# Kernel tuning notes

Hardware: AMD Instinct MI355X
Metric: run time of the kernel (lower is better)

Reference implementation:

```python
import jax, jax.numpy as jnp
import numpy as np
import math

B, T = 16, 60
N_CLASSES = 80
N_ANCHORS = 3
N_CH = 5 + N_CLASSES
STRIDES = (8, 16, 32)
IMG = 608
ANCHORS = np.array([[12,16],[19,36],[40,28],[36,75],[76,55],[72,146],[142,110],[192,243],[459,401]], dtype=np.float32)
IGNORE_THRE = 0.5


def _clip_log(x):
    # torch F.binary_cross_entropy clamps log at -100
    return jnp.maximum(jnp.log(x), -100.0)


def _bce_sum(p, t, w=None):
    l = -(t * _clip_log(p) + (1.0 - t) * _clip_log(1.0 - p))
    if w is not None:
        l = l * w
    return jnp.sum(l)


def _ciou_wh(wh_a, wh_b):
    # truth boxes are xyxy [0,0,w,h]; wh_a [B,T,2], wh_b [9,2] -> CIoU [B,T,9]
    wa = wh_a[..., 0:1]; ha = wh_a[..., 1:2]
    wb = wh_b[:, 0];     hb = wh_b[:, 1]
    iw = jnp.minimum(wa, wb); ih = jnp.minimum(ha, hb)
    en = ((iw > 0) & (ih > 0)).astype(wh_a.dtype)
    area_i = iw * ih * en
    area_u = wa * ha + wb * hb - area_i
    iou = area_i / area_u
    c2 = jnp.maximum(wa, wb) ** 2 + jnp.maximum(ha, hb) ** 2 + 1e-16
    rho2 = ((wa - wb) ** 2 + (ha - hb) ** 2) / 4.0
    v = (4.0 / math.pi ** 2) * (jnp.arctan(wa / ha) - jnp.arctan(wb / hb)) ** 2
    alpha = v / (1.0 - iou + v)
    return iou - (rho2 / c2 + v * alpha)


def _iou_xywh(pred, truth):
    # pred [B,N,4] (cx,cy,w,h), truth [B,T,4] -> IoU [B,N,T]
    p_xy = pred[:, :, None, :2]; p_wh = pred[:, :, None, 2:]
    t_xy = truth[:, None, :, :2]; t_wh = truth[:, None, :, 2:]
    tl = jnp.maximum(p_xy - p_wh * 0.5, t_xy - t_wh * 0.5)
    br = jnp.minimum(p_xy + p_wh * 0.5, t_xy + t_wh * 0.5)
    en = jnp.all(tl < br, axis=-1).astype(pred.dtype)
    area_i = jnp.prod(br - tl, axis=-1) * en
    area_p = pred[..., 2] * pred[..., 3]
    area_t = truth[..., 2] * truth[..., 3]
    return area_i / (area_p[:, :, None] + area_t[:, None, :] - area_i)


def _level_losses(x, labels, oid):
    dt = x.dtype
    stride = STRIDES[oid]
    fsize = IMG // stride
    Bsz = x.shape[0]
    out = x.reshape(Bsz, N_ANCHORS, N_CH, fsize, fsize).transpose(0, 1, 3, 4, 2)  # [B,A,F,F,C]
    sig = jax.nn.sigmoid(out)
    sxy, raw_wh, sobj, scls = sig[..., :2], out[..., 2:4], sig[..., 4], sig[..., 5:]

    all_anch = jnp.asarray(ANCHORS / stride, dt)           # [9,2] grid units
    masked_anch = all_anch[3 * oid: 3 * oid + 3]           # [3,2]
    g = jnp.arange(fsize, dtype=dt)
    px = sxy[..., 0] + g[None, None, None, :]
    py = sxy[..., 1] + g[None, None, :, None]
    pw = jnp.exp(raw_wh[..., 0]) * masked_anch[:, 0][None, :, None, None]
    ph = jnp.exp(raw_wh[..., 1]) * masked_anch[:, 1][None, :, None, None]
    pred = jnp.stack([px, py, pw, ph], axis=-1)            # [B,A,F,F,4]

    lab = jax.lax.stop_gradient(labels.astype(dt))         # targets carry no grad (as in torch)
    valid = jnp.sum(lab, axis=-1) > 0                      # [B,T]
    tx = (lab[..., 2] + lab[..., 0]) / (stride * 2.0)
    ty = (lab[..., 3] + lab[..., 1]) / (stride * 2.0)
    tw = (lab[..., 2] - lab[..., 0]) / stride
    th = (lab[..., 3] - lab[..., 1]) / stride
    ii = jnp.clip(tx.astype(jnp.int32), 0, fsize - 1)      # int16 trunc in torch, coords >= 0
    jj = jnp.clip(ty.astype(jnp.int32), 0, fsize - 1)

    ciou = _ciou_wh(jnp.stack([tw, th], -1), all_anch)     # [B,T,9]
    ciou = jnp.where(valid[..., None], ciou, -1e9)
    best_all = jnp.argmax(ciou, axis=-1)                   # [B,T]
    best_n = best_all % 3
    best_mask = (best_all // 3 == oid) & valid             # anchor owned by this level
    has_match = jnp.any(best_mask, axis=1)                 # [B]; torch `continue` if none

    truth_box = jnp.stack([tx, ty, tw, th], -1) * valid[..., None].astype(dt)
    ious = _iou_xywh(jax.lax.stop_gradient(pred).reshape(Bsz, -1, 4), truth_box)
    ious = jnp.where(valid[:, None, :], ious, 0.0)
    ignore = (jnp.max(ious, axis=-1) > IGNORE_THRE).reshape(Bsz, N_ANCHORS, fsize, fsize)
    obj_mask = jnp.where(has_match[:, None, None, None], 1.0 - ignore.astype(dt), jnp.asarray(1.0, dt))

    # scatter positive assignments; dummy batch row Bsz absorbs masked-out writes
    bidx = jnp.where(best_mask, jnp.arange(Bsz, dtype=jnp.int32)[:, None], Bsz)
    pad1 = lambda a: jnp.concatenate([a, jnp.zeros((1,) + a.shape[1:], a.dtype)], 0)
    obj_mask = pad1(obj_mask).at[bidx, best_n, jj, ii].set(1.0)[:Bsz]
    tgt_mask = jnp.zeros((Bsz + 1, N_ANCHORS, fsize, fsize, 4 + N_CLASSES), dt).at[bidx, best_n, jj, ii].set(1.0)[:Bsz]
    scale = jnp.sqrt(2.0 - tw * th / float(fsize * fsize))  # [B,T]
    tgt_scale = jnp.zeros((Bsz + 1, N_ANCHORS, fsize, fsize, 2), dt).at[bidx, best_n, jj, ii].set(
        jnp.broadcast_to(scale[..., None], scale.shape + (2,)))[:Bsz]
    aw = masked_anch[best_n, 0]; ah = masked_anch[best_n, 1]
    vec = jnp.concatenate([
        (tx - jnp.trunc(tx))[..., None],
        (ty - jnp.trunc(ty))[..., None],
        jnp.log(tw / aw + 1e-16)[..., None],
        jnp.log(th / ah + 1e-16)[..., None],
        jnp.ones_like(tx)[..., None],
        jax.nn.one_hot(lab[..., 4].astype(jnp.int32), N_CLASSES, dtype=dt),
    ], axis=-1)                                            # [B,T,N_CH]
    target = jnp.zeros((Bsz + 1, N_ANCHORS, fsize, fsize, N_CH), dt).at[bidx, best_n, jj, ii].set(vec)[:Bsz]

    o_xy = sxy * tgt_mask[..., :2]
    o_wh = raw_wh * tgt_mask[..., 2:4] * tgt_scale
    o_obj = sobj * obj_mask
    o_cls = scls * tgt_mask[..., 4:]
    t_xy = target[..., :2] * tgt_mask[..., :2]
    t_wh = target[..., 2:4] * tgt_mask[..., 2:4] * tgt_scale
    t_obj = target[..., 4] * obj_mask
    t_cls = target[..., 5:] * tgt_mask[..., 4:]

    l_xy = _bce_sum(o_xy, t_xy, tgt_scale * tgt_scale)
    l_wh = 0.5 * jnp.sum((o_wh - t_wh) ** 2)
    l_obj = _bce_sum(o_obj, t_obj)
    l_cls = _bce_sum(o_cls, t_cls)
    l_l2 = (jnp.sum((o_xy - t_xy) ** 2) + jnp.sum((o_wh - t_wh) ** 2)
            + jnp.sum((o_obj - t_obj) ** 2) + jnp.sum((o_cls - t_cls) ** 2))
    return l_xy, l_wh, l_obj, l_cls, l_l2


def setup_inputs() -> dict:
    key = jax.random.key(0)
    ks = jax.random.split(key, 8)
    x0 = jax.random.normal(ks[0], (B, N_ANCHORS * N_CH, 76, 76), jnp.float32)
    x1 = jax.random.normal(ks[1], (B, N_ANCHORS * N_CH, 38, 38), jnp.float32)
    x2 = jax.random.normal(ks[2], (B, N_ANCHORS * N_CH, 19, 19), jnp.float32)
    cx = jax.random.uniform(ks[3], (B, T), minval=70.0, maxval=538.0)
    cy = jax.random.uniform(ks[4], (B, T), minval=70.0, maxval=538.0)
    bw = jax.random.uniform(ks[5], (B, T), minval=8.0, maxval=128.0)
    bh = jax.random.uniform(ks[6], (B, T), minval=8.0, maxval=128.0)
    cls = jax.random.randint(ks[7], (B, T), 0, N_CLASSES).astype(jnp.float32)
    labels = jnp.stack([cx - bw / 2, cy - bh / 2, cx + bw / 2, cy + bh / 2, cls], axis=-1)
    nvalid = jax.random.randint(jax.random.fold_in(key, 99), (B,), 5, T + 1)
    mask = (jnp.arange(T)[None, :] < nvalid[:, None]).astype(jnp.float32)
    labels = labels * mask[..., None]  # zero padding rows (nlabel = rows with sum>0)
    return {"x0": x0, "x1": x1, "x2": x2, "labels": labels}


def reference(x0, x1, x2, labels):
    totals = [jnp.asarray(0.0, x0.dtype)] * 5
    for oid, x in enumerate((x0, x1, x2)):
        parts = _level_losses(x, labels, oid)
        totals = [a + b for a, b in zip(totals, parts)]
    l_xy, l_wh, l_obj, l_cls, l_l2 = totals
    loss = l_xy + l_wh + l_obj + l_cls
    return loss, l_xy, l_wh, l_obj, l_cls, l_l2
```

## Files before the change

kernel.cpp:

```cpp
#include <hip/hip_runtime.h>

#define BATCH 16
#define TT 60
#define NCLS 80
#define NB0 68
#define NB1 17
#define NB2 5
#define NBX (NB0 + NB1 + NB2)
#define NBLK (NBX * BATCH)

__constant__ float c_aw[9] = {12.f,19.f,40.f,36.f,76.f,72.f,142.f,192.f,459.f};
__constant__ float c_ah[9] = {16.f,36.f,28.f,75.f,55.f,146.f,110.f,243.f,401.f};

__device__ __forceinline__ float sigf(float x){ return 1.0f/(1.0f+expf(-x)); }
__device__ __forceinline__ float clogf_(float x){ return fmaxf(logf(x), -100.0f); }
__device__ __forceinline__ float bcef(float p, float t){
    return -(t*clogf_(p) + (1.0f-t)*clogf_(1.0f-p));
}

__global__ __launch_bounds__(256) void main_kernel(
    const float* __restrict__ x0, const float* __restrict__ x1,
    const float* __restrict__ x2, const float* __restrict__ labels,
    float* __restrict__ ws)
{
    const int bx = blockIdx.x, b = blockIdx.y, tid = threadIdx.x;
    int lvl, lb, fs;
    const float* x;
    if (bx < NB0)            { lvl = 0; lb = bx;             x = x0; fs = 76; }
    else if (bx < NB0 + NB1) { lvl = 1; lb = bx - NB0;       x = x1; fs = 38; }
    else                     { lvl = 2; lb = bx - NB0 - NB1; x = x2; fs = 19; }
    const float stride = (float)(8 << lvl);
    const float invs = 1.0f/stride;
    const int fs2 = fs*fs;
    const int ncell = 3*fs2;
    const int lin = lb*256 + tid;

    __shared__ float  s_atan[9];
    __shared__ float4 s_box[TT];
    __shared__ int    s_mcell[TT], s_mcls[TT];
    __shared__ float  s_vx[TT], s_vy[TT], s_vw[TT], s_vh[TT], s_sc[TT];
    __shared__ int    s_nv, s_nm, s_qn;
    __shared__ int    s_qoff[TT], s_qcls[TT];

    float v0=0,v1=0,v2=0,v3=0,v4=0;
    int a=0, rem=0, ci=0, cj=0;
    if (lin < ncell) {
        a = lin/fs2; rem = lin - a*fs2; cj = rem/fs; ci = rem - cj*fs;
        const float* xb = x + ((size_t)b*255 + a*85)*(size_t)fs2 + rem;
        v0 = xb[0];
        v1 = xb[(size_t)fs2];
        v2 = xb[(size_t)2*fs2];
        v3 = xb[(size_t)3*fs2];
        v4 = xb[(size_t)4*fs2];
    }
    float l0=0,l1=0,l2=0,l3=0,l4=0;
    if (tid < TT) {
        const float* lab = labels + ((size_t)b*TT + tid)*5;
        l0=lab[0]; l1=lab[1]; l2=lab[2]; l3=lab[3]; l4=lab[4];
    }
    if (tid < 9) s_atan[tid] = atanf(c_aw[tid]/c_ah[tid]);
    if (tid == 0) s_qn = 0;
    __syncthreads();

    if (tid < 64) {
        bool valid=false, best=false;
        float tx=0,ty=0,tw=0,th=0;
        int best_all=0;
        if (tid < TT) {
            valid = ((((l0+l1)+l2)+l3)+l4) > 0.0f;
            tx = (l2+l0)*(0.5f*invs);
            ty = (l3+l1)*(0.5f*invs);
            tw = (l2-l0)*invs;
            th = (l3-l1)*invs;
            if (valid) {
                float ta = atanf(tw/th);
                float twth = tw*th;
                float bestv = 0.0f;
                for (int k=0;k<9;k++){
                    float wb=c_aw[k]*invs, hb=c_ah[k]*invs;
                    float iw=fminf(tw,wb), ih=fminf(th,hb);
                    float en=(iw>0.f && ih>0.f)?1.f:0.f;
                    float ai=iw*ih*en;
                    float au=twth+wb*hb-ai;
                    float iou=ai/au;
                    float mw=fmaxf(tw,wb), mh=fmaxf(th,hb);
                    float c2=mw*mw+mh*mh+1e-16f;
                    float rho2=((tw-wb)*(tw-wb)+(th-hb)*(th-hb))*0.25f;
                    float da=ta-s_atan[k];
                    float v=0.40528473456935109f*da*da;
                    float alpha=v/((1.f-iou)+v);
                    float cv=iou-(rho2/c2+v*alpha);
                    if (k==0 || cv>bestv){ bestv=cv; best_all=k; }
                }
            }
        }
        int bn = best_all % 3;
        best = valid && ((best_all/3) == lvl);
        unsigned long long vm = __ballot(valid);
        unsigned long long bm = __ballot(best);
        unsigned long long below = (tid==0) ? 0ULL : ((1ULL<<tid)-1ULL);
        if (valid){
            int r = __popcll(vm & below);
            s_box[r] = make_float4(tx-0.5f*tw, ty-0.5f*th, tx+0.5f*tw, ty+0.5f*th);
        }
        if (best){
            int r = __popcll(bm & below);
            int ti=(int)tx, tj=(int)ty;
            int ii = ti<0?0:(ti>fs-1?fs-1:ti);
            int jj = tj<0?0:(tj>fs-1?fs-1:tj);
            s_mcell[r] = (bn*fs+jj)*fs+ii;
            s_mcls[r]  = (int)l4;
            s_sc[r]    = sqrtf(2.f - tw*th/(float)(fs*fs));
            s_vx[r]    = tx - truncf(tx);
            s_vy[r]    = ty - truncf(ty);
            float aw = c_aw[3*lvl+bn]*invs, ah = c_ah[3*lvl+bn]*invs;
            s_vw[r]    = logf(tw/aw + 1e-16f);
            s_vh[r]    = logf(th/ah + 1e-16f);
        }
        if (tid==0){ s_nv = __popcll(vm); s_nm = __popcll(bm); }
    }
    __syncthreads();

    const int nv = s_nv, nm = s_nm;
    float lxy=0.f, lwh=0.f, lobj=0.f, lcls=0.f, ll2=0.f;
    if (lin < ncell) {
        const float sx = sigf(v0), sy = sigf(v1), sobj = sigf(v4);
        const float aw = c_aw[3*lvl+a]*invs, ah = c_ah[3*lvl+a]*invs;
        const float px = sx + (float)ci;
        const float py = sy + (float)cj;
        const float pw = expf(v2)*aw;
        const float ph = expf(v3)*ah;
        const float area_p = pw*ph;

        int mt = -1;
        for (int k=0;k<nm;k++) if (s_mcell[k] == lin) mt = k;

        bool ign = false;
        if (nm > 0 && mt < 0) {
            const float pxl = px-0.5f*pw, pxr = px+0.5f*pw;
            const float pyl = py-0.5f*ph, pyr = py+0.5f*ph;
            #pragma unroll 4
            for (int t=0;t<nv;t++){
                float4 tb = s_box[t];
                float w = fminf(pxr,tb.z) - fmaxf(pxl,tb.x);
                float h = fminf(pyr,tb.w) - fmaxf(pyl,tb.y);
                float at2 = (tb.z-tb.x)*(tb.w-tb.y);
                ign = ign || ((w>0.f)&&(h>0.f)&&(3.f*(w*h) > area_p+at2));
            }
        }
        float om = (nm>0) ? (ign ? 0.f : 1.f) : 1.f;
        float t4 = 0.f;
        if (mt >= 0){ om = 1.f; t4 = 1.f; }
        const float oo = sobj*om, to = t4*om;
        lobj = bcef(oo, to);
        const float d = oo - to;
        ll2 = d*d;
        if (mt >= 0) {
            const float sc = s_sc[mt], w2 = sc*sc;
            const float mvx = s_vx[mt], mvy = s_vy[mt];
            lxy = w2*(bcef(sx,mvx) + bcef(sy,mvy));
            const float dx = sx-mvx, dy = sy-mvy;
            const float dw = sc*(v2 - s_vw[mt]);
            const float dh = sc*(v3 - s_vh[mt]);
            lwh = 0.5f*(dw*dw + dh*dh);
            ll2 += dx*dx + dy*dy + dw*dw + dh*dh;
            int qi = atomicAdd(&s_qn, 1);
            s_qoff[qi] = (a*85+5)*fs2 + rem;
            s_qcls[qi] = s_mcls[mt];
        }
    }
    __syncthreads();

    const int wid = tid>>6, ln = tid&63;
    const int qn = s_qn;
    for (int it = wid; it < qn; it += 4){
        const size_t base = (size_t)b*255*(size_t)fs2 + (size_t)s_qoff[it];
        const int cc = s_qcls[it];
        float p = sigf(x[base + (size_t)ln*fs2]);
        float tt = (ln==cc) ? 1.f : 0.f;
        lcls += bcef(p, tt);
        float dd = p - tt; ll2 += dd*dd;
        if (ln < NCLS-64) {
            int c = 64+ln;
            p = sigf(x[base + (size_t)c*fs2]);
            tt = (c==cc) ? 1.f : 0.f;
            lcls += bcef(p, tt);
            dd = p - tt; ll2 += dd*dd;
        }
    }

    for (int off=32; off>0; off>>=1){
        lxy  += __shfl_down(lxy,  off);
        lwh  += __shfl_down(lwh,  off);
        lobj += __shfl_down(lobj, off);
        lcls += __shfl_down(lcls, off);
        ll2  += __shfl_down(ll2,  off);
    }
    __shared__ float red[4][5];
    if (ln == 0){ red[wid][0]=lxy; red[wid][1]=lwh; red[wid][2]=lobj; red[wid][3]=lcls; red[wid][4]=ll2; }
    __syncthreads();
    if (tid == 0){
        const int blk = b*NBX + bx;
        ws[0*NBLK + blk] = red[0][0]+red[1][0]+red[2][0]+red[3][0];
        ws[1*NBLK + blk] = red[0][1]+red[1][1]+red[2][1]+red[3][1];
        ws[2*NBLK + blk] = red[0][2]+red[1][2]+red[2][2]+red[3][2];
        ws[3*NBLK + blk] = red[0][3]+red[1][3]+red[2][3]+red[3][3];
        ws[4*NBLK + blk] = red[0][4]+red[1][4]+red[2][4]+red[3][4];
    }
}

__global__ __launch_bounds__(256) void fin_kernel(const float* __restrict__ ws, float* __restrict__ out){
    const int tid = threadIdx.x;
    float s[5] = {0.f,0.f,0.f,0.f,0.f};
    for (int i = tid; i < NBLK; i += 256){
        #pragma unroll
        for (int c=0;c<5;c++) s[c] += ws[c*NBLK + i];
    }
    for (int off=32; off>0; off>>=1){
        #pragma unroll
        for (int c=0;c<5;c++) s[c] += __shfl_down(s[c], off);
    }
    __shared__ float red[4][5];
    const int wid = tid >> 6, ln = tid & 63;
    if (ln == 0){ for (int c=0;c<5;c++) red[wid][c] = s[c]; }
    __syncthreads();
    if (tid == 0){
        float t_xy  = red[0][0]+red[1][0]+red[2][0]+red[3][0];
        float t_wh  = red[0][1]+red[1][1]+red[2][1]+red[3][1];
        float t_obj = red[0][2]+red[1][2]+red[2][2]+red[3][2];
        float t_cls = red[0][3]+red[1][3]+red[2][3]+red[3][3];
        float t_l2  = red[0][4]+red[1][4]+red[2][4]+red[3][4];
        out[0] = t_xy + t_wh + t_obj + t_cls;
        out[1] = t_xy; out[2] = t_wh; out[3] = t_obj; out[4] = t_cls; out[5] = t_l2;
    }
}

extern "C" void kernel_launch(void* const* d_in, const int* in_sizes, int n_in,
                              void* d_out, int out_size, void* d_ws, size_t ws_size,
                              hipStream_t stream) {
    const float* x0 = (const float*)d_in[0];
    const float* x1 = (const float*)d_in[1];
    const float* x2 = (const float*)d_in[2];
    const float* labels = (const float*)d_in[3];
    float* out = (float*)d_out;
    float* ws = (float*)d_ws;

    main_kernel<<<dim3(NBX, BATCH), 256, 0, stream>>>(x0, x1, x2, labels, ws);
    fin_kernel<<<1, 256, 0, stream>>>(ws, out);
}
```

Before: 28.57 us.

## Process two cells per thread and fuse final reduction via last-block atomics

Each thread now handles two grid cells, which halves the block count and amortises the per-block label matching and shared-memory setup over twice as many cells. The separate finalize kernel is replaced by float atomics into the workspace plus a last-block counter that writes the outputs, with a memset to zero the accumulators. This trades a kernel launch for a memset and float atomic ordering. Float atomics make the summation order nondeterministic, and the ignore loop now also runs for matched cells.

Result: slower. 72.53 us (+153.9%).

```diff
diff --git a/kernel.cpp b/kernel.cpp
--- a/kernel.cpp
+++ b/kernel.cpp
@@ -3,11 +3,11 @@
 #define BATCH 16
 #define TT 60
 #define NCLS 80
-#define NB0 68
-#define NB1 17
-#define NB2 5
+#define NB0 34
+#define NB1 9
+#define NB2 3
 #define NBX (NB0 + NB1 + NB2)
-#define NBLK (NBX * BATCH)
+#define NBLK_TOT (NBX * BATCH)
 
 __constant__ float c_aw[9] = {12.f,19.f,40.f,36.f,76.f,72.f,142.f,192.f,459.f};
 __constant__ float c_ah[9] = {16.f,36.f,28.f,75.f,55.f,146.f,110.f,243.f,401.f};
@@ -21,7 +21,7 @@
 __global__ __launch_bounds__(256) void main_kernel(
     const float* __restrict__ x0, const float* __restrict__ x1,
     const float* __restrict__ x2, const float* __restrict__ labels,
-    float* __restrict__ ws)
+    float* __restrict__ ws, float* __restrict__ out)
 {
     const int bx = blockIdx.x, b = blockIdx.y, tid = threadIdx.x;
     int lvl, lb, fs;
@@ -29,29 +29,32 @@
     if (bx < NB0)            { lvl = 0; lb = bx;             x = x0; fs = 76; }
     else if (bx < NB0 + NB1) { lvl = 1; lb = bx - NB0;       x = x1; fs = 38; }
     else                     { lvl = 2; lb = bx - NB0 - NB1; x = x2; fs = 19; }
-    const float stride = (float)(8 << lvl);
-    const float invs = 1.0f/stride;
+    const float invs = 1.0f/(float)(8 << lvl);
     const int fs2 = fs*fs;
     const int ncell = 3*fs2;
-    const int lin = lb*256 + tid;
+    const int lin0 = lb*512 + tid;
+    const int lin1 = lin0 + 256;
 
     __shared__ float  s_atan[9];
     __shared__ float4 s_box[TT];
     __shared__ int    s_mcell[TT], s_mcls[TT];
     __shared__ float  s_vx[TT], s_vy[TT], s_vw[TT], s_vh[TT], s_sc[TT];
-    __shared__ int    s_nv, s_nm, s_qn;
+    __shared__ int    s_nv, s_nm, s_qn, s_last;
     __shared__ int    s_qoff[TT], s_qcls[TT];
 
-    float v0=0,v1=0,v2=0,v3=0,v4=0;
-    int a=0, rem=0, ci=0, cj=0;
-    if (lin < ncell) {
-        a = lin/fs2; rem = lin - a*fs2; cj = rem/fs; ci = rem - cj*fs;
-        const float* xb = x + ((size_t)b*255 + a*85)*(size_t)fs2 + rem;
-        v0 = xb[0];
-        v1 = xb[(size_t)fs2];
-        v2 = xb[(size_t)2*fs2];
-        v3 = xb[(size_t)3*fs2];
-        v4 = xb[(size_t)4*fs2];
+    float v0a=0,v1a=0,v2a=0,v3a=0,v4a=0, v0b=0,v1b=0,v2b=0,v3b=0,v4b=0;
+    int a0=0,rem0=0,ci0=0,cj0=0, a1=0,rem1=0,ci1=0,cj1=0;
+    if (lin0 < ncell) {
+        a0 = lin0/fs2; rem0 = lin0 - a0*fs2; cj0 = rem0/fs; ci0 = rem0 - cj0*fs;
+        const float* xb = x + ((size_t)b*255 + a0*85)*(size_t)fs2 + rem0;
+        v0a = xb[0]; v1a = xb[(size_t)fs2]; v2a = xb[(size_t)2*fs2];
+        v3a = xb[(size_t)3*fs2]; v4a = xb[(size_t)4*fs2];
+    }
+    if (lin1 < ncell) {
+        a1 = lin1/fs2; rem1 = lin1 - a1*fs2; cj1 = rem1/fs; ci1 = rem1 - cj1*fs;
+        const float* xb = x + ((size_t)b*255 + a1*85)*(size_t)fs2 + rem1;
+        v0b = xb[0]; v1b = xb[(size_t)fs2]; v2b = xb[(size_t)2*fs2];
+        v3b = xb[(size_t)3*fs2]; v4b = xb[(size_t)4*fs2];
     }
     float l0=0,l1=0,l2=0,l3=0,l4=0;
     if (tid < TT) {
@@ -123,50 +126,84 @@
 
     const int nv = s_nv, nm = s_nm;
     float lxy=0.f, lwh=0.f, lobj=0.f, lcls=0.f, ll2=0.f;
-    if (lin < ncell) {
-        const float sx = sigf(v0), sy = sigf(v1), sobj = sigf(v4);
-        const float aw = c_aw[3*lvl+a]*invs, ah = c_ah[3*lvl+a]*invs;
-        const float px = sx + (float)ci;
-        const float py = sy + (float)cj;
-        const float pw = expf(v2)*aw;
-        const float ph = expf(v3)*ah;
-        const float area_p = pw*ph;
-
-        int mt = -1;
-        for (int k=0;k<nm;k++) if (s_mcell[k] == lin) mt = k;
-
-        bool ign = false;
-        if (nm > 0 && mt < 0) {
-            const float pxl = px-0.5f*pw, pxr = px+0.5f*pw;
-            const float pyl = py-0.5f*ph, pyr = py+0.5f*ph;
+    const bool c0 = (lin0 < ncell), c1 = (lin1 < ncell);
+    if (c0 | c1) {
+        const float sxa = sigf(v0a), sya = sigf(v1a), soa = sigf(v4a);
+        const float sxb = sigf(v0b), syb = sigf(v1b), sob = sigf(v4b);
+        const float awa = c_aw[3*lvl+a0]*invs, aha = c_ah[3*lvl+a0]*invs;
+        const float awb = c_aw[3*lvl+a1]*invs, ahb = c_ah[3*lvl+a1]*invs;
+        const float pxa = sxa + (float)ci0, pya = sya + (float)cj0;
+        const float pxb = sxb + (float)ci1, pyb = syb + (float)cj1;
+        const float pwa = expf(v2a)*awa, pha = expf(v3a)*aha;
+        const float pwb = expf(v2b)*awb, phb = expf(v3b)*ahb;
+        const float apa = pwa*pha, apb = pwb*phb;
+
+        int mt0 = -1, mt1 = -1;
+        for (int k=0;k<nm;k++){
+            int mc = s_mcell[k];
+            if (mc == lin0) mt0 = k;
+            if (mc == lin1) mt1 = k;
+        }
+
+        bool iga = false, igb = false;
+        if (nm > 0) {
+            const float xla = pxa-0.5f*pwa, xra = pxa+0.5f*pwa;
+            const float yla = pya-0.5f*pha, yra = pya+0.5f*pha;
+            const float xlb = pxb-0.5f*pwb, xrb = pxb+0.5f*pwb;
+            const float ylb = pyb-0.5f*phb, yrb = pyb+0.5f*phb;
             #pragma unroll 4
             for (int t=0;t<nv;t++){
                 float4 tb = s_box[t];
-                float w = fminf(pxr,tb.z) - fmaxf(pxl,tb.x);
-                float h = fminf(pyr,tb.w) - fmaxf(pyl,tb.y);
                 float at2 = (tb.z-tb.x)*(tb.w-tb.y);
-                ign = ign || ((w>0.f)&&(h>0.f)&&(3.f*(w*h) > area_p+at2));
-            }
-        }
-        float om = (nm>0) ? (ign ? 0.f : 1.f) : 1.f;
-        float t4 = 0.f;
-        if (mt >= 0){ om = 1.f; t4 = 1.f; }
-        const float oo = sobj*om, to = t4*om;
-        lobj = bcef(oo, to);
-        const float d = oo - to;
-        ll2 = d*d;
-        if (mt >= 0) {
-            const float sc = s_sc[mt], w2 = sc*sc;
-            const float mvx = s_vx[mt], mvy = s_vy[mt];
-            lxy = w2*(bcef(sx,mvx) + bcef(sy,mvy));
-            const float dx = sx-mvx, dy = sy-mvy;
-            const float dw = sc*(v2 - s_vw[mt]);
-            const float dh = sc*(v3 - s_vh[mt]);
-            lwh = 0.5f*(dw*dw + dh*dh);
-            ll2 += dx*dx + dy*dy + dw*dw + dh*dh;
-            int qi = atomicAdd(&s_qn, 1);
-            s_qoff[qi] = (a*85+5)*fs2 + rem;
-            s_qcls[qi] = s_mcls[mt];
+                float wa = fminf(xra,tb.z) - fmaxf(xla,tb.x);
+                float ha = fminf(yra,tb.w) - fmaxf(yla,tb.y);
+                float wb = fminf(xrb,tb.z) - fmaxf(xlb,tb.x);
+                float hb = fminf(yrb,tb.w) - fmaxf(ylb,tb.y);
+                iga = iga || ((wa>0.f)&&(ha>0.f)&&(3.f*(wa*ha) > apa+at2));
+                igb = igb || ((wb>0.f)&&(hb>0.f)&&(3.f*(wb*hb) > apb+at2));
+            }
+        }
+        if (c0) {
+            float om = (nm>0) ? (iga ? 0.f : 1.f) : 1.f;
+            float t4 = 0.f;
+            if (mt0 >= 0){ om = 1.f; t4 = 1.f; }
+            float oo = soa*om, to = t4*om;
+            lobj += bcef(oo, to);
+            float d = oo - to; ll2 += d*d;
+            if (mt0 >= 0) {
+                float sc = s_sc[mt0], w2 = sc*sc;
+                float mvx = s_vx[mt0], mvy = s_vy[mt0];
+                lxy += w2*(bcef(sxa,mvx) + bcef(sya,mvy));
+                float dx = sxa-mvx, dy = sya-mvy;
+                float dw = sc*(v2a - s_vw[mt0]);
+                float dh = sc*(v3a - s_vh[mt0]);
+                lwh += 0.5f*(dw*dw + dh*dh);
+                ll2 += dx*dx + dy*dy + dw*dw + dh*dh;
+                int qi = atomicAdd(&s_qn, 1);
+                s_qoff[qi] = (a0*85+5)*fs2 + rem0;
+                s_qcls[qi] = s_mcls[mt0];
+            }
+        }
+        if (c1) {
+            float om = (nm>0) ? (igb ? 0.f : 1.f) : 1.f;
+            float t4 = 0.f;
+            if (mt1 >= 0){ om = 1.f; t4 = 1.f; }
+            float oo = sob*om, to = t4*om;
+            lobj += bcef(oo, to);
+            float d = oo - to; ll2 += d*d;
+            if (mt1 >= 0) {
+                float sc = s_sc[mt1], w2 = sc*sc;
+                float mvx = s_vx[mt1], mvy = s_vy[mt1];
+                lxy += w2*(bcef(sxb,mvx) + bcef(syb,mvy));
+                float dx = sxb-mvx, dy = syb-mvy;
+                float dw = sc*(v2b - s_vw[mt1]);
+                float dh = sc*(v3b - s_vh[mt1]);
+                lwh += 0.5f*(dw*dw + dh*dh);
+                ll2 += dx*dx + dy*dy + dw*dw + dh*dh;
+                int qi = atomicAdd(&s_qn, 1);
+                s_qoff[qi] = (a1*85+5)*fs2 + rem1;
+                s_qcls[qi] = s_mcls[mt1];
+            }
         }
     }
     __syncthreads();
@@ -200,36 +237,22 @@
     if (ln == 0){ red[wid][0]=lxy; red[wid][1]=lwh; red[wid][2]=lobj; red[wid][3]=lcls; red[wid][4]=ll2; }
     __syncthreads();
     if (tid == 0){
-        const int blk = b*NBX + bx;
-        ws[0*NBLK + blk] = red[0][0]+red[1][0]+red[2][0]+red[3][0];
-        ws[1*NBLK + blk] = red[0][1]+red[1][1]+red[2][1]+red[3][1];
-        ws[2*NBLK + blk] = red[0][2]+red[1][2]+red[2][2]+red[3][2];
-        ws[3*NBLK + blk] = red[0][3]+red[1][3]+red[2][3]+red[3][3];
-        ws[4*NBLK + blk] = red[0][4]+red[1][4]+red[2][4]+red[3][4];
-    }
-}
-
-__global__ __launch_bounds__(256) void fin_kernel(const float* __restrict__ ws, float* __restrict__ out){
-    const int tid = threadIdx.x;
-    float s[5] = {0.f,0.f,0.f,0.f,0.f};
-    for (int i = tid; i < NBLK; i += 256){
-        #pragma unroll
-        for (int c=0;c<5;c++) s[c] += ws[c*NBLK + i];
-    }
-    for (int off=32; off>0; off>>=1){
-        #pragma unroll
-        for (int c=0;c<5;c++) s[c] += __shfl_down(s[c], off);
-    }
-    __shared__ float red[4][5];
-    const int wid = tid >> 6, ln = tid & 63;
-    if (ln == 0){ for (int c=0;c<5;c++) red[wid][c] = s[c]; }
-    __syncthreads();
-    if (tid == 0){
-        float t_xy  = red[0][0]+red[1][0]+red[2][0]+red[3][0];
-        float t_wh  = red[0][1]+red[1][1]+red[2][1]+red[3][1];
-        float t_obj = red[0][2]+red[1][2]+red[2][2]+red[3][2];
-        float t_cls = red[0][3]+red[1][3]+red[2][3]+red[3][3];
-        float t_l2  = red[0][4]+red[1][4]+red[2][4]+red[3][4];
+        atomicAdd(&ws[0], red[0][0]+red[1][0]+red[2][0]+red[3][0]);
+        atomicAdd(&ws[1], red[0][1]+red[1][1]+red[2][1]+red[3][1]);
+        atomicAdd(&ws[2], red[0][2]+red[1][2]+red[2][2]+red[3][2]);
+        atomicAdd(&ws[3], red[0][3]+red[1][3]+red[2][3]+red[3][3]);
+        atomicAdd(&ws[4], red[0][4]+red[1][4]+red[2][4]+red[3][4]);
+        __threadfence();
+        unsigned int old = atomicAdd((unsigned int*)ws + 8, 1u);
+        s_last = (old == (unsigned int)(NBLK_TOT - 1)) ? 1 : 0;
+    }
+    __syncthreads();
+    if (s_last && tid == 0){
+        float t_xy  = atomicAdd(&ws[0], 0.0f);
+        float t_wh  = atomicAdd(&ws[1], 0.0f);
+        float t_obj = atomicAdd(&ws[2], 0.0f);
+        float t_cls = atomicAdd(&ws[3], 0.0f);
+        float t_l2  = atomicAdd(&ws[4], 0.0f);
         out[0] = t_xy + t_wh + t_obj + t_cls;
         out[1] = t_xy; out[2] = t_wh; out[3] = t_obj; out[4] = t_cls; out[5] = t_l2;
     }
@@ -245,6 +268,6 @@
     float* out = (float*)d_out;
     float* ws = (float*)d_ws;
 
-    main_kernel<<<dim3(NBX, BATCH), 256, 0, stream>>>(x0, x1, x2, labels, ws);
-    fin_kernel<<<1, 256, 0, stream>>>(ws, out);
+    hipMemsetAsync(ws, 0, 64, stream);
+    main_kernel<<<dim3(NBX, BATCH), 256, 0, stream>>>(x0, x1, x2, labels, ws, out);
 }
```
